# Optimization experiments

Hardware: AMD Instinct MI355X
Metric: run time of the kernel (lower is better)

## Reference

```python
import jax, jax.numpy as jnp
import numpy as np

D_IN = 1024
D_OUT = 1024
B, S = 4, 2048

def setup_inputs() -> dict:
    key = jax.random.key(0)
    ks = jax.random.split(key, 7)
    s_in = 1.0 / np.sqrt(D_IN)
    return {
        "X": jax.random.normal(ks[0], (B, S, D_IN), dtype=jnp.float32),
        "Wq": jax.random.uniform(ks[1], (D_OUT, D_IN), jnp.float32, -s_in, s_in),
        "bq": jax.random.uniform(ks[2], (D_OUT,), jnp.float32, -s_in, s_in),
        "Wk": jax.random.uniform(ks[3], (D_OUT, D_IN), jnp.float32, -s_in, s_in),
        "bk": jax.random.uniform(ks[4], (D_OUT,), jnp.float32, -s_in, s_in),
        "Wv": jax.random.uniform(ks[5], (D_OUT, D_IN), jnp.float32, -s_in, s_in),
        "bv": jax.random.uniform(ks[6], (D_OUT,), jnp.float32, -s_in, s_in),
    }

def reference(X, Wq, bq, Wk, bk, Wv, bv):
    # Linear projections (torch Linear: x @ W.T + b)
    q = X @ Wq.T + bq            # [B, S, D_OUT]
    k = X @ Wk.T + bk
    v = X @ Wv.T + bv
    scores = jnp.einsum("bqd,bkd->bqk", q, k) / jnp.sqrt(jnp.float32(D_OUT))
    seq = scores.shape[-1]
    causal = jnp.tril(jnp.ones((seq, seq), dtype=bool))  # True where allowed
    scores = jnp.where(causal, scores, -jnp.inf)
    attn = jax.nn.softmax(scores, axis=-1)
    return jnp.einsum("bqk,bkd->bqd", attn, v)
```

## Files before the change

kernel.cpp:

```cpp
#include <hip/hip_runtime.h>
#include <hip/hip_bf16.h>
#include <hip/hip_fp8.h>


typedef __attribute__((ext_vector_type(8))) short short8;
typedef __attribute__((ext_vector_type(4))) float floatx4;
typedef __attribute__((ext_vector_type(2))) long longx2;

#define SEQ   2048
#define DMODEL 1024
#define NBATCH 4
#define MTOT  (SEQ * NBATCH)

__device__ __forceinline__ void stage16(const void* g, void* l)
{
  __builtin_amdgcn_global_load_lds(
      (const __attribute__((address_space(1))) void*)g,
      (__attribute__((address_space(3))) void*)l, 16, 0, 0);
}

__device__ __forceinline__ unsigned short bf16_bits(float f)
{
  __hip_bfloat16 h = __float2bfloat16(f);
  return *(unsigned short*)&h;
}

__device__ __forceinline__ unsigned char fp8_bits(float f)
{
  __hip_fp8_e4m3 h(f);
  return h.__x;
}

__global__ __launch_bounds__(256) void convert_all(
    const float* __restrict__ X,  const float* __restrict__ Wq,
    const float* __restrict__ Wk, const float* __restrict__ Wv,
    __hip_bfloat16* __restrict__ Xb,  __hip_bfloat16* __restrict__ Wqb,
    __hip_bfloat16* __restrict__ Wkb, __hip_bfloat16* __restrict__ Wvb)
{
  const int b = blockIdx.x;
  const float* src; __hip_bfloat16* dst; int rel;
  if (b < 8192)       { src = X;  dst = Xb;  rel = b; }
  else if (b < 9216)  { src = Wq; dst = Wqb; rel = b - 8192; }
  else if (b < 10240) { src = Wk; dst = Wkb; rel = b - 9216; }
  else                { src = Wv; dst = Wvb; rel = b - 10240; }
  const int i = rel * 1024 + threadIdx.x * 4;
  float4 f = *(const float4*)(src + i);
  uint2 o;
  o.x = (unsigned)bf16_bits(f.x) | ((unsigned)bf16_bits(f.y) << 16);
  o.y = (unsigned)bf16_bits(f.z) | ((unsigned)bf16_bits(f.w) << 16);
  *(uint2*)(dst + i) = o;
}

__global__ __launch_bounds__(256, 2) void gemm_qkv_fused(
    const __hip_bfloat16* __restrict__ Xb,
    const __hip_bfloat16* __restrict__ Wqb,
    const __hip_bfloat16* __restrict__ Wkb,
    const __hip_bfloat16* __restrict__ Wvb,
    const float* __restrict__ bq, const float* __restrict__ bk, const float* __restrict__ bv,
    unsigned char* __restrict__ Qb, unsigned char* __restrict__ Kb,
    __hip_bfloat16* __restrict__ Vt)
{
  __shared__ __hip_bfloat16 As[128 * 32];
  __shared__ __hip_bfloat16 Bs[3][128 * 32];
  const int m0 = blockIdx.y * 128, n0 = blockIdx.x * 128;
  const int tid  = threadIdx.x;
  const int lane = tid & 63;
  const int wave = tid >> 6;
  const int quad = lane >> 4;
  const int r    = lane & 15;
  const int wm   = (wave >> 1) * 64;
  const int wn   = (wave & 1) * 64;
  const int srow = wave * 16 + (lane >> 2);
  const int scol = (lane & 3) * 8;

  const __hip_bfloat16* Wp[3] = {Wqb, Wkb, Wvb};

  __hip_bfloat16* lA0 = As + wave * 512;
  __hip_bfloat16* lA1 = As + 2048 + wave * 512;

  const __hip_bfloat16* aR0 = Xb + (size_t)(m0 + srow) * DMODEL + scol;
  const __hip_bfloat16* aR1 = aR0 + (size_t)64 * DMODEL;

  floatx4 acc[3][4][4] = {};

  for (int kt = 0; kt < DMODEL / 32; ++kt) {
    const int k0 = kt * 32;
    stage16(aR0 + k0, lA0);
    stage16(aR1 + k0, lA1);
#pragma unroll
    for (int w = 0; w < 3; ++w) {
      stage16(Wp[w] + (size_t)(n0 + srow) * DMODEL + scol + k0,      Bs[w] + wave * 512);
      stage16(Wp[w] + (size_t)(n0 + 64 + srow) * DMODEL + scol + k0, Bs[w] + 2048 + wave * 512);
    }
    __syncthreads();
    short8 a[4];
#pragma unroll
    for (int i = 0; i < 4; ++i)
      a[i] = *(const short8*)(As + (wm + i * 16 + r) * 32 + quad * 8);
#pragma unroll
    for (int w = 0; w < 3; ++w) {
      short8 b[4];
#pragma unroll
      for (int j = 0; j < 4; ++j)
        b[j] = *(const short8*)(Bs[w] + (wn + j * 16 + r) * 32 + quad * 8);
#pragma unroll
      for (int i = 0; i < 4; ++i)
#pragma unroll
        for (int j = 0; j < 4; ++j)
          acc[w][i][j] = __builtin_amdgcn_mfma_f32_16x16x32_bf16(a[i], b[j], acc[w][i][j], 0, 0, 0);
    }
    __syncthreads();
  }

  {
    unsigned char* Op[2] = {Qb, Kb};
    const float* Bp[2] = {bq, bk};
#pragma unroll
    for (int w = 0; w < 2; ++w) {
      unsigned char* out = Op[w];
#pragma unroll
      for (int j = 0; j < 4; ++j) {
        const int n = n0 + wn + j * 16 + r;
        const float bb = Bp[w][n];
#pragma unroll
        for (int i = 0; i < 4; ++i) {
          const int mbase = m0 + wm + i * 16 + quad * 4;
#pragma unroll
          for (int e = 0; e < 4; ++e)
            out[(size_t)(mbase + e) * DMODEL + n] = fp8_bits(acc[w][i][j][e] + bb);
        }
      }
    }
  }
  {
    const int z    = m0 >> 11;
    const int posb = (m0 & (SEQ - 1)) + wm;
    __hip_bfloat16* vt = Vt + (size_t)z * DMODEL * SEQ;
#pragma unroll
    for (int j = 0; j < 4; ++j) {
      const int n = n0 + wn + j * 16 + r;
      const float bb = bv[n];
#pragma unroll
      for (int i = 0; i < 4; ++i) {
        const int pos = posb + i * 16 + quad * 4;
        unsigned long long pk =
            (unsigned long long)bf16_bits(acc[2][i][j][0] + bb)
          | ((unsigned long long)bf16_bits(acc[2][i][j][1] + bb) << 16)
          | ((unsigned long long)bf16_bits(acc[2][i][j][2] + bb) << 32)
          | ((unsigned long long)bf16_bits(acc[2][i][j][3] + bb) << 48);
        *(unsigned long long*)(vt + (size_t)n * SEQ + pos) = pk;
      }
    }
  }
}

__device__ __forceinline__ void gemm_core_4w_fp8(
    const unsigned char* __restrict__ A,
    const unsigned char* __restrict__ B,
    int K, int m0, int n0, int kchunks,
    unsigned char* As , unsigned char* Bs ,
    floatx4 acc[4][4])
{
  const int tid  = threadIdx.x;
  const int lane = tid & 63;
  const int wave = tid >> 6;
  const int quad = lane >> 4;
  const int r    = lane & 15;
  const int wm   = (wave >> 1) * 64;
  const int wn   = (wave & 1) * 64;
  const int lrow = lane >> 2;
  const int lcol = (lane & 3) * 16;

  const unsigned char* aB = A + (size_t)(m0 + wave * 32 + lrow) * K + lcol;
  const unsigned char* bB = B + (size_t)(n0 + wave * 32 + lrow) * K + lcol;
  unsigned char* lA = As + wave * 2048;
  unsigned char* lB = Bs + wave * 2048;

  for (int kt = 0; kt < kchunks; ++kt) {
    const int k0 = kt * 64;
#pragma unroll
    for (int s = 0; s < 2; ++s) {
      stage16(aB + (size_t)(16 * s) * K + k0, lA + s * 1024);
      stage16(bB + (size_t)(16 * s) * K + k0, lB + s * 1024);
    }
    __syncthreads();
    longx2 a[4], b[4];
#pragma unroll
    for (int i = 0; i < 4; ++i) {
      a[i] = __builtin_bit_cast(longx2, *(const int4*)(As + (wm + i * 16 + r) * 64 + quad * 16));
      b[i] = __builtin_bit_cast(longx2, *(const int4*)(Bs + (wn + i * 16 + r) * 64 + quad * 16));
    }
#pragma unroll
    for (int kk = 0; kk < 2; ++kk)
#pragma unroll
      for (int i = 0; i < 4; ++i)
#pragma unroll
        for (int j = 0; j < 4; ++j)
          acc[i][j] = __builtin_amdgcn_mfma_f32_16x16x32_fp8_fp8(
              a[i][kk], b[j][kk], acc[i][j], 0, 0, 0);
    __syncthreads();
  }
}

template <bool SUMS>
__device__ __forceinline__ void gemm_core_4w(
    const __hip_bfloat16* __restrict__ A,
    const __hip_bfloat16* __restrict__ B,
    int K, int m0, int n0, int kchunks,
    __hip_bfloat16* As , __hip_bfloat16* Bs ,
    floatx4 acc[4][4], floatx4 acc_s[4])
{
  const int tid  = threadIdx.x;
  const int lane = tid & 63;
  const int wave = tid >> 6;
  const int quad = lane >> 4;
  const int r    = lane & 15;
  const int wm   = (wave >> 1) * 64;
  const int wn   = (wave & 1) * 64;
  const int lrow = lane >> 2;
  const int lcol = (lane & 3) * 8;

  short8 ones;
#pragma unroll
  for (int t = 0; t < 8; ++t) ones[t] = (short)0x3F80;

  const __hip_bfloat16* aB = A + (size_t)(m0 + wave * 32 + lrow) * K + lcol;
  const __hip_bfloat16* bB = B + (size_t)(n0 + wave * 32 + lrow) * K + lcol;
  __hip_bfloat16* lA = As + wave * 1024;
  __hip_bfloat16* lB = Bs + wave * 1024;

  for (int kt = 0; kt < kchunks; ++kt) {
    const int k0 = kt * 32;
#pragma unroll
    for (int s = 0; s < 2; ++s) {
      stage16(aB + (size_t)(16 * s) * K + k0, lA + s * 512);
      stage16(bB + (size_t)(16 * s) * K + k0, lB + s * 512);
    }
    __syncthreads();
    short8 a[4], b[4];
#pragma unroll
    for (int i = 0; i < 4; ++i) {
      a[i] = *(const short8*)(As + (wm + i * 16 + r) * 32 + quad * 8);
      b[i] = *(const short8*)(Bs + (wn + i * 16 + r) * 32 + quad * 8);
    }
    if (SUMS) {
#pragma unroll
      for (int i = 0; i < 4; ++i)
        acc_s[i] = __builtin_amdgcn_mfma_f32_16x16x32_bf16(a[i], ones, acc_s[i], 0, 0, 0);
    }
#pragma unroll
    for (int i = 0; i < 4; ++i)
#pragma unroll
      for (int j = 0; j < 4; ++j)
        acc[i][j] = __builtin_amdgcn_mfma_f32_16x16x32_bf16(a[i], b[j], acc[i][j], 0, 0, 0);
    __syncthreads();
  }
}

__global__ __launch_bounds__(256, 2) void gemm_scores(
    const unsigned char* __restrict__ Qb, const unsigned char* __restrict__ Kb,
    __hip_bfloat16* __restrict__ Sb)
{
  const int b    = blockIdx.x;
  const int orig = (b & 7) * 68 + (b >> 3);
  const int z    = orig / 136;
  const int L    = orig - z * 136;
  int mt = (int)((sqrtf(8.0f * (float)L + 1.0f) - 1.0f) * 0.5f);
  while ((mt + 1) * (mt + 2) / 2 <= L) ++mt;
  while (mt * (mt + 1) / 2 > L) --mt;
  const int nt = L - mt * (mt + 1) / 2;
  const int m0 = mt * 128, n0 = nt * 128;

  __shared__ __align__(16) unsigned char As[128 * 64];
  __shared__ __align__(16) unsigned char Bs[128 * 64];
  const unsigned char* A = Qb + (size_t)z * SEQ * DMODEL;
  const unsigned char* B = Kb + (size_t)z * SEQ * DMODEL;
  __hip_bfloat16* outp = Sb + (size_t)z * SEQ * SEQ;
  floatx4 acc[4][4] = {};
  gemm_core_4w_fp8(A, B, DMODEL, m0, n0, DMODEL / 64, As, Bs, acc);

  const int lane = threadIdx.x & 63, wave = threadIdx.x >> 6;
  const int quad = lane >> 4, r = lane & 15;
  const int wm = (wave >> 1) * 64, wn = (wave & 1) * 64;
  const float scale = 0.03125f;
#pragma unroll
  for (int i = 0; i < 4; ++i) {
    const int mbase = m0 + wm + i * 16 + quad * 4;
#pragma unroll
    for (int e = 0; e < 4; ++e) {
      const int row = mbase + e;
#pragma unroll
      for (int j = 0; j < 4; ++j) {
        const int n = n0 + wn + j * 16 + r;
        const float pv = (n <= row) ? __expf(acc[i][j][e] * scale) : 0.f;
        outp[(size_t)row * SEQ + n] = __float2bfloat16(pv);
      }
    }
  }
}

__global__ __launch_bounds__(256, 2) void gemm_pv(
    const __hip_bfloat16* __restrict__ Sb, const __hip_bfloat16* __restrict__ Vt,
    float* __restrict__ Out)
{
  const int b    = blockIdx.x;
  const int xcd  = b & 7;
  const int slot = b >> 3;
  const int gi   = slot >> 3;
  const int q    = gi * 8 + xcd;
  const int n0   = (slot & 7) * 128;
  const int z    = q & 3;
  const int mt   = 15 - (q >> 2);
  const int m0   = mt * 128;

  __shared__ __align__(16) __hip_bfloat16 As[128 * 32];
  __shared__ __align__(16) __hip_bfloat16 Bs[128 * 32];
  const __hip_bfloat16* A = Sb + (size_t)z * SEQ * SEQ;
  const __hip_bfloat16* B = Vt + (size_t)z * DMODEL * SEQ;
  float* outp = Out + (size_t)z * SEQ * DMODEL;

  floatx4 acc[4][4] = {};
  floatx4 acc_s[4] = {};
  const int kchunks = 4 * mt + 4;
  gemm_core_4w<true>(A, B, SEQ, m0, n0, kchunks, As, Bs, acc, acc_s);

  const int lane = threadIdx.x & 63, wave = threadIdx.x >> 6;
  const int quad = lane >> 4, r = lane & 15;
  const int wm = (wave >> 1) * 64, wn = (wave & 1) * 64;
#pragma unroll
  for (int i = 0; i < 4; ++i) {
    const int mbase = m0 + wm + i * 16 + quad * 4;
    float inv[4];
#pragma unroll
    for (int e = 0; e < 4; ++e) inv[e] = 1.f / acc_s[i][e];
#pragma unroll
    for (int j = 0; j < 4; ++j) {
      const int n = n0 + wn + j * 16 + r;
#pragma unroll
      for (int e = 0; e < 4; ++e)
        outp[(size_t)(mbase + e) * DMODEL + n] = acc[i][j][e] * inv[e];
    }
  }
}

extern "C" void kernel_launch(void* const* d_in, const int* in_sizes, int n_in,
                              void* d_out, int out_size, void* d_ws, size_t ws_size,
                              hipStream_t stream)
{
  const float* X  = (const float*)d_in[0];
  const float* Wq = (const float*)d_in[1];
  const float* bq = (const float*)d_in[2];
  const float* Wk = (const float*)d_in[3];
  const float* bk = (const float*)d_in[4];
  const float* Wv = (const float*)d_in[5];
  const float* bv = (const float*)d_in[6];
  float* Out = (float*)d_out;

  char* ws = (char*)d_ws;
  size_t off = 0;
  auto alloc = [&](size_t bytes) -> void* {
    void* p = ws + off;
    off += (bytes + 255) & ~(size_t)255;
    return p;
  };
  __hip_bfloat16* Xb  = (__hip_bfloat16*)alloc((size_t)MTOT * DMODEL * 2);
  __hip_bfloat16* Wqb = (__hip_bfloat16*)alloc((size_t)DMODEL * DMODEL * 2);
  __hip_bfloat16* Wkb = (__hip_bfloat16*)alloc((size_t)DMODEL * DMODEL * 2);
  __hip_bfloat16* Wvb = (__hip_bfloat16*)alloc((size_t)DMODEL * DMODEL * 2);
  unsigned char*  Qb  = (unsigned char*)alloc((size_t)MTOT * DMODEL);
  unsigned char*  Kb  = (unsigned char*)alloc((size_t)MTOT * DMODEL);
  __hip_bfloat16* Vt  = (__hip_bfloat16*)alloc((size_t)MTOT * DMODEL * 2);
  __hip_bfloat16* Sb  = (__hip_bfloat16*)alloc((size_t)NBATCH * SEQ * SEQ * 2);
  (void)ws_size; (void)in_sizes; (void)n_in; (void)out_size;

  convert_all<<<11264, 256, 0, stream>>>(X, Wq, Wk, Wv, Xb, Wqb, Wkb, Wvb);
  gemm_qkv_fused<<<dim3(DMODEL / 128, MTOT / 128), 256, 0, stream>>>(
      Xb, Wqb, Wkb, Wvb, bq, bk, bv, Qb, Kb, Vt);
  gemm_scores<<<dim3(544), 256, 0, stream>>>(Qb, Kb, Sb);
  gemm_pv<<<dim3(512), 256, 0, stream>>>(Sb, Vt, Out);
}
```

Measured before the change: 219.0 us.

## Rewrite QKV GEMM with 8-wave, 4-stage pipelined LDS ring buffer

Replaces the QKV projection GEMM with a 512-thread kernel that treats the three weight tiles as one 128x384 B tile. It uses a 4-deep LDS ring buffer and global_load_lds prefetch three steps ahead, with manual vmcnt/lgkmcnt waits, raw s_barriers and s_setprio around the MFMA bursts. The block index is swizzled so neighbouring blocks share weight tiles for L2 reuse. The goal is to overlap global loads with MFMA work, which the old version serialized with two __syncthreads per k-step. The trade-off is much higher LDS use (128 KB) and fragile hand-tuned wait counts.

```diff
diff --git a/kernel.cpp b/kernel.cpp
--- a/kernel.cpp
+++ b/kernel.cpp
@@ -11,6 +11,10 @@
 #define DMODEL 1024
 #define NBATCH 4
 #define MTOT  (SEQ * NBATCH)
+
+#define BARRIER() asm volatile("s_barrier" ::: "memory")
+#define LGKM0() do { asm volatile("s_waitcnt lgkmcnt(0)" ::: "memory"); \
+                     __builtin_amdgcn_sched_barrier(0); } while (0)
 
 __device__ __forceinline__ void stage16(const void* g, void* l)
 {
@@ -51,7 +55,65 @@
   *(uint2*)(dst + i) = o;
 }
 
-__global__ __launch_bounds__(256, 2) void gemm_qkv_fused(
+template <int ENDW, bool STG>
+__device__ __forceinline__ void qkv_tile_step(
+    int t,
+    __hip_bfloat16 (*ASb)[128 * 32], __hip_bfloat16 (*BSb)[384 * 32],
+    const __hip_bfloat16* __restrict__ aSrc,
+    const __hip_bfloat16* __restrict__ bSrc0,
+    const __hip_bfloat16* __restrict__ bSrc1,
+    const __hip_bfloat16* __restrict__ bSrc2,
+    int wave, int wr, int wc, int quad, int r,
+    floatx4 (&acc)[4][6])
+{
+  const __hip_bfloat16* As_ = ASb[t & 3];
+  const __hip_bfloat16* Bs_ = BSb[t & 3];
+  short8 a_[4], b_[3];
+#pragma unroll
+  for (int i = 0; i < 4; ++i)
+    a_[i] = *(const short8*)(As_ + (wr * 64 + i * 16 + r) * 32 + quad * 8);
+#pragma unroll
+  for (int j = 0; j < 3; ++j)
+    b_[j] = *(const short8*)(Bs_ + (wc * 96 + j * 16 + r) * 32 + quad * 8);
+  if (STG) {
+    const int tn = t + 3, bn = tn & 3;
+    stage16(aSrc + tn * 32, ASb[bn] + wave * 512);
+    stage16(bSrc0 + tn * 32, BSb[bn] + wave * 512);
+  }
+  BARRIER();
+  LGKM0();
+  __builtin_amdgcn_s_setprio(1);
+#pragma unroll
+  for (int i = 0; i < 4; ++i)
+#pragma unroll
+    for (int j = 0; j < 3; ++j)
+      acc[i][j] = __builtin_amdgcn_mfma_f32_16x16x32_bf16(a_[i], b_[j], acc[i][j], 0, 0, 0);
+  __builtin_amdgcn_s_setprio(0);
+  BARRIER();
+#pragma unroll
+  for (int j = 0; j < 3; ++j)
+    b_[j] = *(const short8*)(Bs_ + (wc * 96 + (j + 3) * 16 + r) * 32 + quad * 8);
+  if (STG) {
+    const int tn = t + 3, bn = tn & 3;
+    stage16(bSrc1 + tn * 32, BSb[bn] + 4096 + wave * 512);
+    stage16(bSrc2 + tn * 32, BSb[bn] + 8192 + wave * 512);
+  }
+  BARRIER();
+  LGKM0();
+  __builtin_amdgcn_s_setprio(1);
+#pragma unroll
+  for (int i = 0; i < 4; ++i)
+#pragma unroll
+    for (int j = 0; j < 3; ++j)
+      acc[i][j + 3] = __builtin_amdgcn_mfma_f32_16x16x32_bf16(a_[i], b_[j], acc[i][j + 3], 0, 0, 0);
+  __builtin_amdgcn_s_setprio(0);
+  if (ENDW == 8)      asm volatile("s_waitcnt vmcnt(8)" ::: "memory");
+  else if (ENDW == 4) asm volatile("s_waitcnt vmcnt(4)" ::: "memory");
+  else if (ENDW == 0) asm volatile("s_waitcnt vmcnt(0)" ::: "memory");
+  BARRIER();
+}
+
+__global__ __launch_bounds__(512, 2) void gemm_qkv_8p(
     const __hip_bfloat16* __restrict__ Xb,
     const __hip_bfloat16* __restrict__ Wqb,
     const __hip_bfloat16* __restrict__ Wkb,
@@ -60,94 +122,74 @@
     unsigned char* __restrict__ Qb, unsigned char* __restrict__ Kb,
     __hip_bfloat16* __restrict__ Vt)
 {
-  __shared__ __hip_bfloat16 As[128 * 32];
-  __shared__ __hip_bfloat16 Bs[3][128 * 32];
-  const int m0 = blockIdx.y * 128, n0 = blockIdx.x * 128;
-  const int tid  = threadIdx.x;
-  const int lane = tid & 63;
-  const int wave = tid >> 6;
-  const int quad = lane >> 4;
-  const int r    = lane & 15;
-  const int wm   = (wave >> 1) * 64;
-  const int wn   = (wave & 1) * 64;
-  const int srow = wave * 16 + (lane >> 2);
-  const int scol = (lane & 3) * 8;
-
-  const __hip_bfloat16* Wp[3] = {Wqb, Wkb, Wvb};
-
-  __hip_bfloat16* lA0 = As + wave * 512;
-  __hip_bfloat16* lA1 = As + 2048 + wave * 512;
-
-  const __hip_bfloat16* aR0 = Xb + (size_t)(m0 + srow) * DMODEL + scol;
-  const __hip_bfloat16* aR1 = aR0 + (size_t)64 * DMODEL;
-
-  floatx4 acc[3][4][4] = {};
-
-  for (int kt = 0; kt < DMODEL / 32; ++kt) {
-    const int k0 = kt * 32;
-    stage16(aR0 + k0, lA0);
-    stage16(aR1 + k0, lA1);
-#pragma unroll
-    for (int w = 0; w < 3; ++w) {
-      stage16(Wp[w] + (size_t)(n0 + srow) * DMODEL + scol + k0,      Bs[w] + wave * 512);
-      stage16(Wp[w] + (size_t)(n0 + 64 + srow) * DMODEL + scol + k0, Bs[w] + 2048 + wave * 512);
-    }
-    __syncthreads();
-    short8 a[4];
-#pragma unroll
-    for (int i = 0; i < 4; ++i)
-      a[i] = *(const short8*)(As + (wm + i * 16 + r) * 32 + quad * 8);
-#pragma unroll
-    for (int w = 0; w < 3; ++w) {
-      short8 b[4];
-#pragma unroll
-      for (int j = 0; j < 4; ++j)
-        b[j] = *(const short8*)(Bs[w] + (wn + j * 16 + r) * 32 + quad * 8);
-#pragma unroll
-      for (int i = 0; i < 4; ++i)
-#pragma unroll
-        for (int j = 0; j < 4; ++j)
-          acc[w][i][j] = __builtin_amdgcn_mfma_f32_16x16x32_bf16(a[i], b[j], acc[w][i][j], 0, 0, 0);
-    }
-    __syncthreads();
-  }
-
-  {
-    unsigned char* Op[2] = {Qb, Kb};
-    const float* Bp[2] = {bq, bk};
-#pragma unroll
-    for (int w = 0; w < 2; ++w) {
-      unsigned char* out = Op[w];
-#pragma unroll
-      for (int j = 0; j < 4; ++j) {
-        const int n = n0 + wn + j * 16 + r;
-        const float bb = Bp[w][n];
-#pragma unroll
-        for (int i = 0; i < 4; ++i) {
-          const int mbase = m0 + wm + i * 16 + quad * 4;
-#pragma unroll
-          for (int e = 0; e < 4; ++e)
-            out[(size_t)(mbase + e) * DMODEL + n] = fp8_bits(acc[w][i][j][e] + bb);
-        }
+  __shared__ __hip_bfloat16 ASb[4][128 * 32];
+  __shared__ __hip_bfloat16 BSb[4][384 * 32];
+
+  const int b    = blockIdx.x;
+  const int orig = (b & 7) * 64 + (b >> 3);
+  const int mt = orig >> 3, ng = orig & 7;
+  const int m0 = mt * 128, n0 = ng * 128;
+
+  const int tid = threadIdx.x;
+  const int lane = tid & 63, wave = tid >> 6;
+  const int quad = lane >> 4, r = lane & 15;
+  const int wr = wave >> 2, wc = wave & 3;
+
+  const __hip_bfloat16* aSrc  = Xb  + (size_t)(m0 + (tid >> 2)) * DMODEL + (tid & 3) * 8;
+  const __hip_bfloat16* bSrc0 = Wqb + (size_t)(n0 + (tid >> 2)) * DMODEL + (tid & 3) * 8;
+  const __hip_bfloat16* bSrc1 = Wkb + (size_t)(n0 + (tid >> 2)) * DMODEL + (tid & 3) * 8;
+  const __hip_bfloat16* bSrc2 = Wvb + (size_t)(n0 + (tid >> 2)) * DMODEL + (tid & 3) * 8;
+
+  floatx4 acc[4][6] = {};
+
+#pragma unroll
+  for (int t0 = 0; t0 < 3; ++t0) {
+    stage16(aSrc  + t0 * 32, ASb[t0] + wave * 512);
+    stage16(bSrc0 + t0 * 32, BSb[t0] + wave * 512);
+    stage16(bSrc1 + t0 * 32, BSb[t0] + 4096 + wave * 512);
+    stage16(bSrc2 + t0 * 32, BSb[t0] + 8192 + wave * 512);
+  }
+  asm volatile("s_waitcnt vmcnt(8)" ::: "memory");
+  BARRIER();
+
+  for (int t = 0; t < 29; ++t)
+    qkv_tile_step<8, true>(t, ASb, BSb, aSrc, bSrc0, bSrc1, bSrc2,
+                           wave, wr, wc, quad, r, acc);
+  qkv_tile_step<4, false>(29, ASb, BSb, aSrc, bSrc0, bSrc1, bSrc2,
+                          wave, wr, wc, quad, r, acc);
+  qkv_tile_step<0, false>(30, ASb, BSb, aSrc, bSrc0, bSrc1, bSrc2,
+                          wave, wr, wc, quad, r, acc);
+  qkv_tile_step<-1, false>(31, ASb, BSb, aSrc, bSrc0, bSrc1, bSrc2,
+                           wave, wr, wc, quad, r, acc);
+
+#pragma unroll
+  for (int j = 0; j < 6; ++j) {
+    const int colglob = wc * 96 + j * 16 + r;
+    const int wsel = (wc * 96 + j * 16) >> 7;
+    const int n = n0 + (colglob & 127);
+    if (wsel < 2) {
+      unsigned char* out = wsel ? Kb : Qb;
+      const float bb = (wsel ? bk : bq)[n];
+#pragma unroll
+      for (int i = 0; i < 4; ++i) {
+        const int mb = m0 + wr * 64 + i * 16 + quad * 4;
+#pragma unroll
+        for (int e = 0; e < 4; ++e)
+          out[(size_t)(mb + e) * DMODEL + n] = fp8_bits(acc[i][j][e] + bb);
       }
-    }
-  }
-  {
-    const int z    = m0 >> 11;
-    const int posb = (m0 & (SEQ - 1)) + wm;
-    __hip_bfloat16* vt = Vt + (size_t)z * DMODEL * SEQ;
-#pragma unroll
-    for (int j = 0; j < 4; ++j) {
-      const int n = n0 + wn + j * 16 + r;
+    } else {
+      const int z = m0 >> 11;
+      const int posb0 = (m0 & (SEQ - 1)) + wr * 64;
+      __hip_bfloat16* vt = Vt + (size_t)z * DMODEL * SEQ;
       const float bb = bv[n];
 #pragma unroll
       for (int i = 0; i < 4; ++i) {
-        const int pos = posb + i * 16 + quad * 4;
+        const int pos = posb0 + i * 16 + quad * 4;
         unsigned long long pk =
-            (unsigned long long)bf16_bits(acc[2][i][j][0] + bb)
-          | ((unsigned long long)bf16_bits(acc[2][i][j][1] + bb) << 16)
-          | ((unsigned long long)bf16_bits(acc[2][i][j][2] + bb) << 32)
-          | ((unsigned long long)bf16_bits(acc[2][i][j][3] + bb) << 48);
+            (unsigned long long)bf16_bits(acc[i][j][0] + bb)
+          | ((unsigned long long)bf16_bits(acc[i][j][1] + bb) << 16)
+          | ((unsigned long long)bf16_bits(acc[i][j][2] + bb) << 32)
+          | ((unsigned long long)bf16_bits(acc[i][j][3] + bb) << 48);
         *(unsigned long long*)(vt + (size_t)n * SEQ + pos) = pk;
       }
     }
@@ -374,7 +416,7 @@
   (void)ws_size; (void)in_sizes; (void)n_in; (void)out_size;
 
   convert_all<<<11264, 256, 0, stream>>>(X, Wq, Wk, Wv, Xb, Wqb, Wkb, Wvb);
-  gemm_qkv_fused<<<dim3(DMODEL / 128, MTOT / 128), 256, 0, stream>>>(
+  gemm_qkv_8p<<<512, 512, 0, stream>>>(
       Xb, Wqb, Wkb, Wvb, bq, bk, bv, Qb, Kb, Vt);
   gemm_scores<<<dim3(544), 256, 0, stream>>>(Qb, Kb, Sb);
   gemm_pv<<<dim3(512), 256, 0, stream>>>(Sb, Vt, Out);
```

Result: slower. 224.9 us (+2.7%).

## Double-buffer LDS staging in all three GEMMs and swizzle QKV blocks across XCDs

Applied to the files above, without the earlier changes.

Each GEMM core now keeps two LDS buffers. The global-to-LDS loads for chunk k+1 are issued before the MFMAs on chunk k, with one explicit waitcnt plus barrier per step, so memory latency is meant to overlap with compute. The QKV GEMM moves to a 1D grid remapped so that consecutive blocks on each XCD share X rows, aiming for better L2 reuse. The cost is doubled LDS use, which reaches 64KB per block in the QKV kernel and may lower occupancy below the requested 2 blocks per CU. The full vmcnt(0) wait each step also limits how much overlap is possible.

```diff
diff --git a/kernel.cpp b/kernel.cpp
--- a/kernel.cpp
+++ b/kernel.cpp
@@ -11,6 +11,11 @@
 #define DMODEL 1024
 #define NBATCH 4
 #define MTOT  (SEQ * NBATCH)
+
+#define STEP_FENCE() do {                                              \
+    asm volatile("s_waitcnt vmcnt(0) lgkmcnt(0)" ::: "memory");        \
+    __builtin_amdgcn_sched_barrier(0);                                 \
+    __builtin_amdgcn_s_barrier(); } while (0)
 
 __device__ __forceinline__ void stage16(const void* g, void* l)
 {
@@ -51,7 +56,7 @@
   *(uint2*)(dst + i) = o;
 }
 
-__global__ __launch_bounds__(256, 2) void gemm_qkv_fused(
+__global__ __launch_bounds__(256, 2) void gemm_qkv_db(
     const __hip_bfloat16* __restrict__ Xb,
     const __hip_bfloat16* __restrict__ Wqb,
     const __hip_bfloat16* __restrict__ Wkb,
@@ -60,9 +65,14 @@
     unsigned char* __restrict__ Qb, unsigned char* __restrict__ Kb,
     __hip_bfloat16* __restrict__ Vt)
 {
-  __shared__ __hip_bfloat16 As[128 * 32];
-  __shared__ __hip_bfloat16 Bs[3][128 * 32];
-  const int m0 = blockIdx.y * 128, n0 = blockIdx.x * 128;
+  __shared__ __hip_bfloat16 As[2][128 * 32];
+  __shared__ __hip_bfloat16 Bs[2][3][128 * 32];
+
+  const int b    = blockIdx.x;
+  const int orig = (b & 7) * 64 + (b >> 3);
+  const int mt = orig >> 3, ng = orig & 7;
+  const int m0 = mt * 128, n0 = ng * 128;
+
   const int tid  = threadIdx.x;
   const int lane = tid & 63;
   const int wave = tid >> 6;
@@ -73,43 +83,62 @@
   const int srow = wave * 16 + (lane >> 2);
   const int scol = (lane & 3) * 8;
 
-  const __hip_bfloat16* Wp[3] = {Wqb, Wkb, Wvb};
-
-  __hip_bfloat16* lA0 = As + wave * 512;
-  __hip_bfloat16* lA1 = As + 2048 + wave * 512;
-
   const __hip_bfloat16* aR0 = Xb + (size_t)(m0 + srow) * DMODEL + scol;
   const __hip_bfloat16* aR1 = aR0 + (size_t)64 * DMODEL;
+  const __hip_bfloat16* bR0[3], * bR1[3];
+  {
+    const __hip_bfloat16* Wp[3] = {Wqb, Wkb, Wvb};
+#pragma unroll
+    for (int w = 0; w < 3; ++w) {
+      bR0[w] = Wp[w] + (size_t)(n0 + srow) * DMODEL + scol;
+      bR1[w] = bR0[w] + (size_t)64 * DMODEL;
+    }
+  }
 
   floatx4 acc[3][4][4] = {};
 
-  for (int kt = 0; kt < DMODEL / 32; ++kt) {
-    const int k0 = kt * 32;
-    stage16(aR0 + k0, lA0);
-    stage16(aR1 + k0, lA1);
+  {
+    stage16(aR0, As[0] + wave * 512);
+    stage16(aR1, As[0] + 2048 + wave * 512);
 #pragma unroll
     for (int w = 0; w < 3; ++w) {
-      stage16(Wp[w] + (size_t)(n0 + srow) * DMODEL + scol + k0,      Bs[w] + wave * 512);
-      stage16(Wp[w] + (size_t)(n0 + 64 + srow) * DMODEL + scol + k0, Bs[w] + 2048 + wave * 512);
-    }
-    __syncthreads();
+      stage16(bR0[w], Bs[0][w] + wave * 512);
+      stage16(bR1[w], Bs[0][w] + 2048 + wave * 512);
+    }
+    asm volatile("s_waitcnt vmcnt(0)" ::: "memory");
+    __builtin_amdgcn_sched_barrier(0);
+    __builtin_amdgcn_s_barrier();
+  }
+
+  for (int kt = 0; kt < 32; ++kt) {
+    const int cur = kt & 1;
+    if (kt < 31) {
+      const int k0 = (kt + 1) * 32, nb = cur ^ 1;
+      stage16(aR0 + k0, As[nb] + wave * 512);
+      stage16(aR1 + k0, As[nb] + 2048 + wave * 512);
+#pragma unroll
+      for (int w = 0; w < 3; ++w) {
+        stage16(bR0[w] + k0, Bs[nb][w] + wave * 512);
+        stage16(bR1[w] + k0, Bs[nb][w] + 2048 + wave * 512);
+      }
+    }
     short8 a[4];
 #pragma unroll
     for (int i = 0; i < 4; ++i)
-      a[i] = *(const short8*)(As + (wm + i * 16 + r) * 32 + quad * 8);
+      a[i] = *(const short8*)(As[cur] + (wm + i * 16 + r) * 32 + quad * 8);
 #pragma unroll
     for (int w = 0; w < 3; ++w) {
-      short8 b[4];
+      short8 bb[4];
 #pragma unroll
       for (int j = 0; j < 4; ++j)
-        b[j] = *(const short8*)(Bs[w] + (wn + j * 16 + r) * 32 + quad * 8);
+        bb[j] = *(const short8*)(Bs[cur][w] + (wn + j * 16 + r) * 32 + quad * 8);
 #pragma unroll
       for (int i = 0; i < 4; ++i)
 #pragma unroll
         for (int j = 0; j < 4; ++j)
-          acc[w][i][j] = __builtin_amdgcn_mfma_f32_16x16x32_bf16(a[i], b[j], acc[w][i][j], 0, 0, 0);
-    }
-    __syncthreads();
+          acc[w][i][j] = __builtin_amdgcn_mfma_f32_16x16x32_bf16(a[i], bb[j], acc[w][i][j], 0, 0, 0);
+    }
+    STEP_FENCE();
   }
 
   {
@@ -154,11 +183,11 @@
   }
 }
 
-__device__ __forceinline__ void gemm_core_4w_fp8(
+__device__ __forceinline__ void gemm_core_4w_fp8_db(
     const unsigned char* __restrict__ A,
     const unsigned char* __restrict__ B,
     int K, int m0, int n0, int kchunks,
-    unsigned char* As , unsigned char* Bs ,
+    unsigned char (*As)[128 * 64], unsigned char (*Bs)[128 * 64],
     floatx4 acc[4][4])
 {
   const int tid  = threadIdx.x;
@@ -173,22 +202,31 @@
 
   const unsigned char* aB = A + (size_t)(m0 + wave * 32 + lrow) * K + lcol;
   const unsigned char* bB = B + (size_t)(n0 + wave * 32 + lrow) * K + lcol;
-  unsigned char* lA = As + wave * 2048;
-  unsigned char* lB = Bs + wave * 2048;
+
+#pragma unroll
+  for (int s = 0; s < 2; ++s) {
+    stage16(aB + (size_t)(16 * s) * K, As[0] + wave * 2048 + s * 1024);
+    stage16(bB + (size_t)(16 * s) * K, Bs[0] + wave * 2048 + s * 1024);
+  }
+  asm volatile("s_waitcnt vmcnt(0)" ::: "memory");
+  __builtin_amdgcn_sched_barrier(0);
+  __builtin_amdgcn_s_barrier();
 
   for (int kt = 0; kt < kchunks; ++kt) {
-    const int k0 = kt * 64;
-#pragma unroll
-    for (int s = 0; s < 2; ++s) {
-      stage16(aB + (size_t)(16 * s) * K + k0, lA + s * 1024);
-      stage16(bB + (size_t)(16 * s) * K + k0, lB + s * 1024);
-    }
-    __syncthreads();
-    longx2 a[4], b[4];
+    const int cur = kt & 1;
+    if (kt + 1 < kchunks) {
+      const int k0 = (kt + 1) * 64, nb = cur ^ 1;
+#pragma unroll
+      for (int s = 0; s < 2; ++s) {
+        stage16(aB + (size_t)(16 * s) * K + k0, As[nb] + wave * 2048 + s * 1024);
+        stage16(bB + (size_t)(16 * s) * K + k0, Bs[nb] + wave * 2048 + s * 1024);
+      }
+    }
+    longx2 a[4], bb[4];
 #pragma unroll
     for (int i = 0; i < 4; ++i) {
-      a[i] = __builtin_bit_cast(longx2, *(const int4*)(As + (wm + i * 16 + r) * 64 + quad * 16));
-      b[i] = __builtin_bit_cast(longx2, *(const int4*)(Bs + (wn + i * 16 + r) * 64 + quad * 16));
+      a[i]  = __builtin_bit_cast(longx2, *(const int4*)(As[cur] + (wm + i * 16 + r) * 64 + quad * 16));
+      bb[i] = __builtin_bit_cast(longx2, *(const int4*)(Bs[cur] + (wn + i * 16 + r) * 64 + quad * 16));
     }
 #pragma unroll
     for (int kk = 0; kk < 2; ++kk)
@@ -197,17 +235,17 @@
 #pragma unroll
         for (int j = 0; j < 4; ++j)
           acc[i][j] = __builtin_amdgcn_mfma_f32_16x16x32_fp8_fp8(
-              a[i][kk], b[j][kk], acc[i][j], 0, 0, 0);
-    __syncthreads();
+              a[i][kk], bb[j][kk], acc[i][j], 0, 0, 0);
+    STEP_FENCE();
   }
 }
 
 template <bool SUMS>
-__device__ __forceinline__ void gemm_core_4w(
+__device__ __forceinline__ void gemm_core_4w_db(
     const __hip_bfloat16* __restrict__ A,
     const __hip_bfloat16* __restrict__ B,
     int K, int m0, int n0, int kchunks,
-    __hip_bfloat16* As , __hip_bfloat16* Bs ,
+    __hip_bfloat16 (*As)[128 * 32], __hip_bfloat16 (*Bs)[128 * 32],
     floatx4 acc[4][4], floatx4 acc_s[4])
 {
   const int tid  = threadIdx.x;
@@ -226,22 +264,31 @@
 
   const __hip_bfloat16* aB = A + (size_t)(m0 + wave * 32 + lrow) * K + lcol;
   const __hip_bfloat16* bB = B + (size_t)(n0 + wave * 32 + lrow) * K + lcol;
-  __hip_bfloat16* lA = As + wave * 1024;
-  __hip_bfloat16* lB = Bs + wave * 1024;
+
+#pragma unroll
+  for (int s = 0; s < 2; ++s) {
+    stage16(aB + (size_t)(16 * s) * K, As[0] + wave * 1024 + s * 512);
+    stage16(bB + (size_t)(16 * s) * K, Bs[0] + wave * 1024 + s * 512);
+  }
+  asm volatile("s_waitcnt vmcnt(0)" ::: "memory");
+  __builtin_amdgcn_sched_barrier(0);
+  __builtin_amdgcn_s_barrier();
 
   for (int kt = 0; kt < kchunks; ++kt) {
-    const int k0 = kt * 32;
-#pragma unroll
-    for (int s = 0; s < 2; ++s) {
-      stage16(aB + (size_t)(16 * s) * K + k0, lA + s * 512);
-      stage16(bB + (size_t)(16 * s) * K + k0, lB + s * 512);
-    }
-    __syncthreads();
-    short8 a[4], b[4];
+    const int cur = kt & 1;
+    if (kt + 1 < kchunks) {
+      const int k0 = (kt + 1) * 32, nb = cur ^ 1;
+#pragma unroll
+      for (int s = 0; s < 2; ++s) {
+        stage16(aB + (size_t)(16 * s) * K + k0, As[nb] + wave * 1024 + s * 512);
+        stage16(bB + (size_t)(16 * s) * K + k0, Bs[nb] + wave * 1024 + s * 512);
+      }
+    }
+    short8 a[4], bb[4];
 #pragma unroll
     for (int i = 0; i < 4; ++i) {
-      a[i] = *(const short8*)(As + (wm + i * 16 + r) * 32 + quad * 8);
-      b[i] = *(const short8*)(Bs + (wn + i * 16 + r) * 32 + quad * 8);
+      a[i]  = *(const short8*)(As[cur] + (wm + i * 16 + r) * 32 + quad * 8);
+      bb[i] = *(const short8*)(Bs[cur] + (wn + i * 16 + r) * 32 + quad * 8);
     }
     if (SUMS) {
 #pragma unroll
@@ -252,8 +299,8 @@
     for (int i = 0; i < 4; ++i)
 #pragma unroll
       for (int j = 0; j < 4; ++j)
-        acc[i][j] = __builtin_amdgcn_mfma_f32_16x16x32_bf16(a[i], b[j], acc[i][j], 0, 0, 0);
-    __syncthreads();
+        acc[i][j] = __builtin_amdgcn_mfma_f32_16x16x32_bf16(a[i], bb[j], acc[i][j], 0, 0, 0);
+    STEP_FENCE();
   }
 }
 
@@ -271,13 +318,13 @@
   const int nt = L - mt * (mt + 1) / 2;
   const int m0 = mt * 128, n0 = nt * 128;
 
-  __shared__ __align__(16) unsigned char As[128 * 64];
-  __shared__ __align__(16) unsigned char Bs[128 * 64];
+  __shared__ __align__(16) unsigned char As[2][128 * 64];
+  __shared__ __align__(16) unsigned char Bs[2][128 * 64];
   const unsigned char* A = Qb + (size_t)z * SEQ * DMODEL;
   const unsigned char* B = Kb + (size_t)z * SEQ * DMODEL;
   __hip_bfloat16* outp = Sb + (size_t)z * SEQ * SEQ;
   floatx4 acc[4][4] = {};
-  gemm_core_4w_fp8(A, B, DMODEL, m0, n0, DMODEL / 64, As, Bs, acc);
+  gemm_core_4w_fp8_db(A, B, DMODEL, m0, n0, DMODEL / 64, As, Bs, acc);
 
   const int lane = threadIdx.x & 63, wave = threadIdx.x >> 6;
   const int quad = lane >> 4, r = lane & 15;
@@ -313,8 +360,8 @@
   const int mt   = 15 - (q >> 2);
   const int m0   = mt * 128;
 
-  __shared__ __align__(16) __hip_bfloat16 As[128 * 32];
-  __shared__ __align__(16) __hip_bfloat16 Bs[128 * 32];
+  __shared__ __align__(16) __hip_bfloat16 As[2][128 * 32];
+  __shared__ __align__(16) __hip_bfloat16 Bs[2][128 * 32];
   const __hip_bfloat16* A = Sb + (size_t)z * SEQ * SEQ;
   const __hip_bfloat16* B = Vt + (size_t)z * DMODEL * SEQ;
   float* outp = Out + (size_t)z * SEQ * DMODEL;
@@ -322,7 +369,7 @@
   floatx4 acc[4][4] = {};
   floatx4 acc_s[4] = {};
   const int kchunks = 4 * mt + 4;
-  gemm_core_4w<true>(A, B, SEQ, m0, n0, kchunks, As, Bs, acc, acc_s);
+  gemm_core_4w_db<true>(A, B, SEQ, m0, n0, kchunks, As, Bs, acc, acc_s);
 
   const int lane = threadIdx.x & 63, wave = threadIdx.x >> 6;
   const int quad = lane >> 4, r = lane & 15;
@@ -374,7 +421,7 @@
   (void)ws_size; (void)in_sizes; (void)n_in; (void)out_size;
 
   convert_all<<<11264, 256, 0, stream>>>(X, Wq, Wk, Wv, Xb, Wqb, Wkb, Wvb);
-  gemm_qkv_fused<<<dim3(DMODEL / 128, MTOT / 128), 256, 0, stream>>>(
+  gemm_qkv_db<<<512, 256, 0, stream>>>(
       Xb, Wqb, Wkb, Wvb, bq, bk, bv, Qb, Kb, Vt);
   gemm_scores<<<dim3(544), 256, 0, stream>>>(Qb, Kb, Sb);
   gemm_pv<<<dim3(512), 256, 0, stream>>>(Sb, Vt, Out);
```

Result: no change. 216.1 us (-1.3%).

## Double-buffer LDS in fused QKV GEMM and remap blocks for XCD locality

Applied to the files above, without the earlier changes.

Converts the fused QKV projection GEMM to a double-buffered LDS pipeline that prefetches the next K-tile while computing MFMAs on the current one, with one barrier per step instead of two. It also launches a 1D grid with a block-index remap so that blocks landing on the same XCD share contiguous M/N tiles, improving L2 reuse. LDS usage doubles to 64 KB per block, which may pressure occupancy at two blocks per CU.

```diff
diff --git a/kernel.cpp b/kernel.cpp
--- a/kernel.cpp
+++ b/kernel.cpp
@@ -11,6 +11,11 @@
 #define DMODEL 1024
 #define NBATCH 4
 #define MTOT  (SEQ * NBATCH)
+
+#define STEP_FENCE() do {                                              \
+    asm volatile("s_waitcnt vmcnt(0) lgkmcnt(0)" ::: "memory");        \
+    __builtin_amdgcn_sched_barrier(0);                                 \
+    __builtin_amdgcn_s_barrier(); } while (0)
 
 __device__ __forceinline__ void stage16(const void* g, void* l)
 {
@@ -51,7 +56,7 @@
   *(uint2*)(dst + i) = o;
 }
 
-__global__ __launch_bounds__(256, 2) void gemm_qkv_fused(
+__global__ __launch_bounds__(256, 2) void gemm_qkv_db(
     const __hip_bfloat16* __restrict__ Xb,
     const __hip_bfloat16* __restrict__ Wqb,
     const __hip_bfloat16* __restrict__ Wkb,
@@ -60,9 +65,14 @@
     unsigned char* __restrict__ Qb, unsigned char* __restrict__ Kb,
     __hip_bfloat16* __restrict__ Vt)
 {
-  __shared__ __hip_bfloat16 As[128 * 32];
-  __shared__ __hip_bfloat16 Bs[3][128 * 32];
-  const int m0 = blockIdx.y * 128, n0 = blockIdx.x * 128;
+  __shared__ __hip_bfloat16 As[2][128 * 32];
+  __shared__ __hip_bfloat16 Bs[2][3][128 * 32];
+
+  const int b    = blockIdx.x;
+  const int orig = (b & 7) * 64 + (b >> 3);
+  const int mt = orig >> 3, ng = orig & 7;
+  const int m0 = mt * 128, n0 = ng * 128;
+
   const int tid  = threadIdx.x;
   const int lane = tid & 63;
   const int wave = tid >> 6;
@@ -73,43 +83,62 @@
   const int srow = wave * 16 + (lane >> 2);
   const int scol = (lane & 3) * 8;
 
-  const __hip_bfloat16* Wp[3] = {Wqb, Wkb, Wvb};
-
-  __hip_bfloat16* lA0 = As + wave * 512;
-  __hip_bfloat16* lA1 = As + 2048 + wave * 512;
-
   const __hip_bfloat16* aR0 = Xb + (size_t)(m0 + srow) * DMODEL + scol;
   const __hip_bfloat16* aR1 = aR0 + (size_t)64 * DMODEL;
+  const __hip_bfloat16* bR0[3], * bR1[3];
+  {
+    const __hip_bfloat16* Wp[3] = {Wqb, Wkb, Wvb};
+#pragma unroll
+    for (int w = 0; w < 3; ++w) {
+      bR0[w] = Wp[w] + (size_t)(n0 + srow) * DMODEL + scol;
+      bR1[w] = bR0[w] + (size_t)64 * DMODEL;
+    }
+  }
 
   floatx4 acc[3][4][4] = {};
 
-  for (int kt = 0; kt < DMODEL / 32; ++kt) {
-    const int k0 = kt * 32;
-    stage16(aR0 + k0, lA0);
-    stage16(aR1 + k0, lA1);
+  {
+    stage16(aR0, As[0] + wave * 512);
+    stage16(aR1, As[0] + 2048 + wave * 512);
 #pragma unroll
     for (int w = 0; w < 3; ++w) {
-      stage16(Wp[w] + (size_t)(n0 + srow) * DMODEL + scol + k0,      Bs[w] + wave * 512);
-      stage16(Wp[w] + (size_t)(n0 + 64 + srow) * DMODEL + scol + k0, Bs[w] + 2048 + wave * 512);
-    }
-    __syncthreads();
+      stage16(bR0[w], Bs[0][w] + wave * 512);
+      stage16(bR1[w], Bs[0][w] + 2048 + wave * 512);
+    }
+    asm volatile("s_waitcnt vmcnt(0)" ::: "memory");
+    __builtin_amdgcn_sched_barrier(0);
+    __builtin_amdgcn_s_barrier();
+  }
+
+  for (int kt = 0; kt < 32; ++kt) {
+    const int cur = kt & 1;
+    if (kt < 31) {
+      const int k0 = (kt + 1) * 32, nb = cur ^ 1;
+      stage16(aR0 + k0, As[nb] + wave * 512);
+      stage16(aR1 + k0, As[nb] + 2048 + wave * 512);
+#pragma unroll
+      for (int w = 0; w < 3; ++w) {
+        stage16(bR0[w] + k0, Bs[nb][w] + wave * 512);
+        stage16(bR1[w] + k0, Bs[nb][w] + 2048 + wave * 512);
+      }
+    }
     short8 a[4];
 #pragma unroll
     for (int i = 0; i < 4; ++i)
-      a[i] = *(const short8*)(As + (wm + i * 16 + r) * 32 + quad * 8);
+      a[i] = *(const short8*)(As[cur] + (wm + i * 16 + r) * 32 + quad * 8);
 #pragma unroll
     for (int w = 0; w < 3; ++w) {
-      short8 b[4];
+      short8 bb[4];
 #pragma unroll
       for (int j = 0; j < 4; ++j)
-        b[j] = *(const short8*)(Bs[w] + (wn + j * 16 + r) * 32 + quad * 8);
+        bb[j] = *(const short8*)(Bs[cur][w] + (wn + j * 16 + r) * 32 + quad * 8);
 #pragma unroll
       for (int i = 0; i < 4; ++i)
 #pragma unroll
         for (int j = 0; j < 4; ++j)
-          acc[w][i][j] = __builtin_amdgcn_mfma_f32_16x16x32_bf16(a[i], b[j], acc[w][i][j], 0, 0, 0);
-    }
-    __syncthreads();
+          acc[w][i][j] = __builtin_amdgcn_mfma_f32_16x16x32_bf16(a[i], bb[j], acc[w][i][j], 0, 0, 0);
+    }
+    STEP_FENCE();
   }
 
   {
@@ -374,7 +403,7 @@
   (void)ws_size; (void)in_sizes; (void)n_in; (void)out_size;
 
   convert_all<<<11264, 256, 0, stream>>>(X, Wq, Wk, Wv, Xb, Wqb, Wkb, Wvb);
-  gemm_qkv_fused<<<dim3(DMODEL / 128, MTOT / 128), 256, 0, stream>>>(
+  gemm_qkv_db<<<512, 256, 0, stream>>>(
       Xb, Wqb, Wkb, Wvb, bq, bk, bv, Qb, Kb, Vt);
   gemm_scores<<<dim3(544), 256, 0, stream>>>(Qb, Kb, Sb);
   gemm_pv<<<dim3(512), 256, 0, stream>>>(Sb, Vt, Out);
```

Result: faster. 214.4 us (-2.1%).
